# Kernel optimization log

Hardware: AMD Instinct MI355X
Metric: run time of the kernel (lower is better)

## Reference

```python
import jax, jax.numpy as jnp
import numpy as np

B, T, N, H, E, LH, OUT, D = 64, 12, 325, 64, 32, 128, 12, 1
META_OFF = 65  # x[..., :1] is the signal, x[..., 65:] is the 32-dim temporal meta input


def _mlp(meta, W1, b1, W2, b2):
    # meta: (B,E); W1: (4,E,LH); W2: (4,LH,O) -> (4,B,O); 4 = gates g,i,f,o
    h = jax.nn.relu(jnp.einsum('be,geh->gbh', meta, W1) + b1[:, None, :])
    return jnp.einsum('gbh,gho->gbo', h, W2) + b2[:, None, :]


def setup_inputs() -> dict:
    key = jax.random.key(0)
    ks = jax.random.split(key, 16)
    s = lambda k, shape: jax.random.normal(k, shape, dtype=jnp.float32) * 0.05
    return {
        'x': jax.random.normal(ks[0], (B, T, N, 1 + 64 + E), dtype=jnp.float32),
        'lwx_W1': s(ks[1], (4, E, LH)), 'lwx_b1': s(ks[2], (4, LH)),
        'lwx_W2': s(ks[3], (4, LH, D * H)), 'lwx_b2': s(ks[4], (4, D * H)),
        'lwh_W1': s(ks[5], (4, E, LH)), 'lwh_b1': s(ks[6], (4, LH)),
        'lwh_W2': s(ks[7], (4, LH, H * H)), 'lwh_b2': s(ks[8], (4, H * H)),
        'lb_W1': s(ks[9], (4, E, LH)), 'lb_b1': s(ks[10], (4, LH)),
        'lb_W2': s(ks[11], (4, LH, H)), 'lb_b2': s(ks[12], (4, H)),
        'fc1_W': s(ks[13], (H, H // 2)), 'fc1_b': jnp.zeros((H // 2,), jnp.float32),
        'fc2_W': s(ks[14], (H // 2, OUT * D)), 'fc2_b': jnp.zeros((OUT * D,), jnp.float32),
    }


def reference(x, lwx_W1, lwx_b1, lwx_W2, lwx_b2,
              lwh_W1, lwh_b1, lwh_W2, lwh_b2,
              lb_W1, lb_b1, lb_W2, lb_b2,
              fc1_W, fc1_b, fc2_W, fc2_b):
    batch = x.shape[0]
    meta = jnp.mean(x[:, :, 0, META_OFF:], axis=1)  # (B,E)
    xs = jnp.transpose(x[..., :D], (1, 0, 2, 3))    # (T,B,N,D)

    Wx = _mlp(meta, lwx_W1, lwx_b1, lwx_W2, lwx_b2).reshape(4, batch, D, H)
    Wh = _mlp(meta, lwh_W1, lwh_b1, lwh_W2, lwh_b2).reshape(4, batch, H, H)
    b = _mlp(meta, lb_W1, lb_b1, lb_W2, lb_b2).reshape(4, batch, 1, H)

    def step(carry, xt):
        h, c = carry
        # (4,B,N,H): per-batch weights -> batched matmuls for all 4 gates
        z = (jnp.einsum('bnd,gbdh->gbnh', xt, Wx)
             + jnp.einsum('bnh,gbhk->gbnk', h, Wh) + b)
        g = jnp.tanh(z[0])
        i = jax.nn.sigmoid(z[1])
        f = jax.nn.sigmoid(z[2])
        o = jax.nn.sigmoid(z[3])
        c = g * i + c * f
        h = jnp.tanh(c) * o
        return (h, c), None

    # h0=c0=0 reproduces the torch t==0 special case exactly
    h0 = jnp.zeros((batch, N, H), x.dtype)
    (h, _), _ = jax.lax.scan(step, (h0, h0), xs)

    out = jax.nn.relu(h)
    out = jax.nn.relu(out @ fc1_W + fc1_b) @ fc2_W + fc2_b  # (B,N,OUT*D)
    out = out.reshape(batch, N, OUT, D)
    return jnp.transpose(out, (0, 2, 1, 3))  # (B,OUT,N,D)
```

## Files before the change

### kernel.cpp

```cpp
#include <hip/hip_runtime.h>
#include <stdint.h>

#define TT 12
#define NN 325
#define HH 64
#define EE 32
#define LHH 128
#define OO 12
#define CIN 97
#define MOFF 65
#define BB 64

typedef __attribute__((ext_vector_type(8))) short bf8;
typedef __attribute__((ext_vector_type(4))) float f4;

__device__ __forceinline__ float sigf(float x) {
  return __builtin_amdgcn_rcpf(1.f + __builtin_amdgcn_exp2f(-1.4426950408889634f * x));
}
__device__ __forceinline__ float tanhfast(float x) {
  return 1.f - 2.f * __builtin_amdgcn_rcpf(1.f + __builtin_amdgcn_exp2f(2.8853900817779268f * x));
}
__device__ __forceinline__ unsigned short f2bf(float f) {
  unsigned int u = __float_as_uint(f);
  u += 0x7fffu + ((u >> 16) & 1u);
  return (unsigned short)(u >> 16);
}
__device__ __forceinline__ float bf2f(unsigned short s) {
  return __uint_as_float(((unsigned int)s) << 16);
}

__global__ __launch_bounds__(256, 2) void k_prep(
    const float* __restrict__ x,
    const float* __restrict__ xw1, const float* __restrict__ xb1,
    const float* __restrict__ xw2, const float* __restrict__ xb2,
    const float* __restrict__ hw1, const float* __restrict__ hb1,
    const float* __restrict__ hw2, const float* __restrict__ hb2,
    const float* __restrict__ bw1, const float* __restrict__ bb1,
    const float* __restrict__ bw2, const float* __restrict__ bb2,
    unsigned short* __restrict__ whb, float* __restrict__ xg,
    float* __restrict__ wx_ws, float* __restrict__ bg_ws)
{
  const int bi = blockIdx.x, tid = threadIdx.x;
  __shared__ float meta_s[BB][EE];
  __shared__ float hs[BB][132];
  __shared__ float w2s[LHH][HH];

  for (int m = tid; m < BB * EE; m += 256) {
    const int b = m >> 5, e = m & 31;
    float s = 0.f;
    #pragma unroll
    for (int t = 0; t < TT; ++t)
      s += x[(size_t)((b * TT + t) * NN) * CIN + MOFF + e];
    meta_s[b][e] = s * (1.f / 12.f);
  }

  if (bi < 256) {
    const int g = bi >> 6, i = bi & 63;

    const int base = bi * 976;
    #pragma unroll
    for (int kk = 0; kk < 4; ++kk) {
      const int flat = base + kk * 256 + tid;
      if (flat < BB * TT * NN) {
        const int b = flat / (TT * NN);
        const int r = flat - b * (TT * NN);
        const int t = r / NN;
        const int n = r - t * NN;
        xg[flat] = x[(size_t)((b * TT + t) * NN + n) * CIN];
      }
    }
    for (int idx = tid; idx < LHH * HH; idx += 256)
      w2s[idx >> 6][idx & 63] = hw2[(size_t)(g * LHH + (idx >> 6)) * 4096 + i * 64 + (idx & 63)];
    __syncthreads();

    for (int m = tid; m < BB * LHH; m += 256) {
      const int b = m >> 7, l = m & 127;
      float a = hb1[g * LHH + l];
      const float* w = hw1 + (size_t)g * (EE * LHH) + l;
      #pragma unroll
      for (int e = 0; e < EE; ++e) a = fmaf(meta_s[b][e], w[e * LHH], a);
      hs[b][l] = fmaxf(a, 0.f);
    }
    __syncthreads();

    const int rg = tid >> 4, cg = tid & 15;
    const int b0 = rg * 4, j0 = cg * 4;
    float acc[4][4] = {};
    for (int l = 0; l < LHH; l += 4) {
      f4 hv[4];
      #pragma unroll
      for (int rr = 0; rr < 4; ++rr) hv[rr] = *(const f4*)&hs[b0 + rr][l];
      #pragma unroll
      for (int ll = 0; ll < 4; ++ll) {
        const f4 wv = *(const f4*)&w2s[l + ll][j0];
        #pragma unroll
        for (int rr = 0; rr < 4; ++rr)
          #pragma unroll
          for (int jj = 0; jj < 4; ++jj)
            acc[rr][jj] = fmaf(hv[rr][ll], wv[jj], acc[rr][jj]);
      }
    }
    const int kh = i >> 5, quad = (i >> 3) & 3, j8 = i & 7;
    #pragma unroll
    for (int rr = 0; rr < 4; ++rr) {
      const int b = b0 + rr;
      #pragma unroll
      for (int jj = 0; jj < 4; ++jj) {
        const int j = j0 + jj;
        const float v = acc[rr][jj] + hb2[g * 4096 + i * 64 + j];
        const int col = g * 64 + j;
        const int nt = col >> 4, c16 = col & 15;
        const int lane = quad * 16 + c16;
        whb[(size_t)((b * 32 + kh * 16 + nt) * 64 + lane) * 8 + j8] = f2bf(v);
      }
    }
  } else {
    const int role = bi - 256;
    const int g = role >> 1;
    const int isb = role & 1;
    const float* W1 = isb ? bw1 : xw1;
    const float* B1 = isb ? bb1 : xb1;
    const float* W2 = isb ? bw2 : xw2;
    const float* B2 = isb ? bb2 : xb2;
    float* dst = isb ? bg_ws : wx_ws;
    __syncthreads();

    for (int m = tid; m < BB * LHH; m += 256) {
      const int b = m >> 7, l = m & 127;
      float a = B1[g * LHH + l];
      const float* w = W1 + (size_t)g * (EE * LHH) + l;
      #pragma unroll
      for (int e = 0; e < EE; ++e) a = fmaf(meta_s[b][e], w[e * LHH], a);
      hs[b][l] = fmaxf(a, 0.f);
    }
    __syncthreads();

    for (int m = tid; m < BB * HH; m += 256) {
      const int b = m >> 6, h = m & 63;
      float a = B2[g * HH + h];
      const float* w = W2 + (size_t)g * (LHH * HH) + h;
      #pragma unroll 8
      for (int l = 0; l < LHH; ++l) a = fmaf(hs[b][l], w[l * HH], a);
      dst[b * 256 + g * 64 + h] = a;
    }
  }
}

__global__ __launch_bounds__(256, 3) void k_lstm(
    const float* __restrict__ xg, const float* __restrict__ wx_ws,
    const float* __restrict__ bg_ws, const unsigned short* __restrict__ whb,
    const float* __restrict__ fc1W, const float* __restrict__ fc1b,
    const float* __restrict__ fc2W, const float* __restrict__ fc2b,
    float* __restrict__ out)
{
  const int rb = blockIdx.x, b = blockIdx.y, tid = threadIdx.x;
  const int wave = tid >> 6, lane = tid & 63, quad = lane >> 4, c16 = lane & 15;
  const int n0 = rb * 32;

  __shared__ __align__(16) unsigned short Hs[2][2][16][72];
  __shared__ float Xs[TT][32];
  __shared__ float fc1s[HH * 32];
  __shared__ float fc2s[32 * OO];
  __shared__ float HIDs[32][36];
  __shared__ float fc1bs[32];
  __shared__ float fc2bs[OO];

  for (int idx = tid; idx < TT * 32; idx += 256) {
    const int t = idx >> 5, r = idx & 31, n = n0 + r;
    Xs[t][r] = (n < NN) ? xg[b * (TT * NN) + t * NN + n] : 0.f;
  }
  for (int idx = tid; idx < HH * 32; idx += 256) fc1s[idx] = fc1W[idx];
  for (int idx = tid; idx < 32 * OO; idx += 256) fc2s[idx] = fc2W[idx];
  if (tid < 32) fc1bs[tid] = fc1b[tid];
  if (tid < OO) fc2bs[tid] = fc2b[tid];

  float wxv[4], bgv[4];
  #pragma unroll
  for (int g = 0; g < 4; ++g) {
    wxv[g] = wx_ws[b * 256 + g * 64 + wave * 16 + c16];
    bgv[g] = bg_ws[b * 256 + g * 64 + wave * 16 + c16];
  }
  bf8 wf[2][4];
  #pragma unroll
  for (int kh = 0; kh < 2; ++kh)
    #pragma unroll
    for (int g = 0; g < 4; ++g)
      wf[kh][g] = *(const bf8*)(whb + (size_t)((b * 32 + kh * 16 + g * 4 + wave) * 64 + lane) * 8);

  float cst[2][4];
  #pragma unroll
  for (int ta = 0; ta < 2; ++ta)
    #pragma unroll
    for (int r = 0; r < 4; ++r) cst[ta][r] = 0.f;

  __syncthreads();

  #pragma unroll 1
  for (int t = 0; t < TT; ++t) {
    bf8 af[2][2];
    if (t > 0) {
      #pragma unroll
      for (int ta = 0; ta < 2; ++ta) {
        af[ta][0] = *(const bf8*)&Hs[(t - 1) & 1][ta][c16][quad * 8];
        af[ta][1] = *(const bf8*)&Hs[(t - 1) & 1][ta][c16][32 + quad * 8];
      }
    }
    f4 ac[2][4];
    #pragma unroll
    for (int ta = 0; ta < 2; ++ta) {
      float xr[4];
      #pragma unroll
      for (int r = 0; r < 4; ++r) xr[r] = Xs[t][ta * 16 + quad * 4 + r];
      #pragma unroll
      for (int g = 0; g < 4; ++g)
        #pragma unroll
        for (int r = 0; r < 4; ++r)
          ac[ta][g][r] = fmaf(xr[r], wxv[g], bgv[g]);
    }
    if (t > 0) {
      #pragma unroll
      for (int ta = 0; ta < 2; ++ta)
        #pragma unroll
        for (int g = 0; g < 4; ++g) {
          ac[ta][g] = __builtin_amdgcn_mfma_f32_16x16x32_bf16(af[ta][0], wf[0][g], ac[ta][g], 0, 0, 0);
          ac[ta][g] = __builtin_amdgcn_mfma_f32_16x16x32_bf16(af[ta][1], wf[1][g], ac[ta][g], 0, 0, 0);
        }
    }
    #pragma unroll
    for (int ta = 0; ta < 2; ++ta)
      #pragma unroll
      for (int r = 0; r < 4; ++r) {
        const float gg = tanhfast(ac[ta][0][r]);
        const float ii = sigf(ac[ta][1][r]);
        const float ff = sigf(ac[ta][2][r]);
        const float oo = sigf(ac[ta][3][r]);
        const float cc = fmaf(gg, ii, cst[ta][r] * ff);
        cst[ta][r] = cc;
        const float hh = tanhfast(cc) * oo;
        Hs[t & 1][ta][quad * 4 + r][wave * 16 + c16] = f2bf(hh);
      }
    __syncthreads();
  }

  {
    const int row32 = tid & 31, uu = tid >> 5;
    const int ta = row32 >> 4, row = row32 & 15;
    float hacc[4];
    #pragma unroll
    for (int j = 0; j < 4; ++j) hacc[j] = fc1bs[uu * 4 + j];
    #pragma unroll
    for (int kc = 0; kc < 8; ++kc) {
      const bf8 hv = *(const bf8*)&Hs[1][ta][row][kc * 8];
      #pragma unroll
      for (int j8 = 0; j8 < 8; ++j8) {
        const float hk = fmaxf(bf2f((unsigned short)hv[j8]), 0.f);
        const int k = kc * 8 + j8;
        #pragma unroll
        for (int j = 0; j < 4; ++j)
          hacc[j] = fmaf(hk, fc1s[k * 32 + uu * 4 + j], hacc[j]);
      }
    }
    #pragma unroll
    for (int j = 0; j < 4; ++j)
      HIDs[row32][uu * 4 + j] = fmaxf(hacc[j], 0.f);
  }
  __syncthreads();
  for (int idx = tid; idx < 32 * OO; idx += 256) {
    const int o = idx >> 5, row32 = idx & 31;
    float a = fc2bs[o];
    #pragma unroll
    for (int k = 0; k < 32; ++k)
      a = fmaf(HIDs[row32][k], fc2s[k * OO + o], a);
    const int n = n0 + row32;
    if (n < NN)
      out[b * (OO * NN) + o * NN + n] = a;
  }
}

extern "C" void kernel_launch(void* const* d_in, const int* in_sizes, int n_in,
                              void* d_out, int out_size, void* d_ws, size_t ws_size,
                              hipStream_t stream) {
  const float* x    = (const float*)d_in[0];
  const float* xw1  = (const float*)d_in[1];
  const float* xb1  = (const float*)d_in[2];
  const float* xw2  = (const float*)d_in[3];
  const float* xb2  = (const float*)d_in[4];
  const float* hw1  = (const float*)d_in[5];
  const float* hb1  = (const float*)d_in[6];
  const float* hw2  = (const float*)d_in[7];
  const float* hb2  = (const float*)d_in[8];
  const float* bw1  = (const float*)d_in[9];
  const float* bb1  = (const float*)d_in[10];
  const float* bw2  = (const float*)d_in[11];
  const float* bb2  = (const float*)d_in[12];
  const float* fc1W = (const float*)d_in[13];
  const float* fc1b = (const float*)d_in[14];
  const float* fc2W = (const float*)d_in[15];
  const float* fc2b = (const float*)d_in[16];
  float* out = (float*)d_out;

  float* ws = (float*)d_ws;
  float* wx_ws = ws;
  float* bg_ws = ws + 16384;
  float* xg_ws = ws + 32768;
  unsigned short* whb = (unsigned short*)(ws + 32768 + BB * TT * NN);

  k_prep<<<264, 256, 0, stream>>>(x, xw1, xb1, xw2, xb2, hw1, hb1, hw2, hb2,
                                  bw1, bb1, bw2, bb2, whb, xg_ws, wx_ws, bg_ws);
  k_lstm<<<dim3(11, 64), 256, 0, stream>>>(xg_ws, wx_ws, bg_ws, whb,
                                           fc1W, fc1b, fc2W, fc2b, out);
}
```

Before: 247.0 us.

## Split prep kernel to compute meta and hidden MLP layers once

The single prep kernel had each of 264 blocks recompute the full batch meta mean (strided reads of x) and the first hidden MLP layer. The work is now split into two kernels. k_meta runs per batch and computes the meta vector, all first-layer hiddens and the small Wx and bias MLPs. k_wh reads the precomputed Wh hiddens from workspace and does only the large second-layer matmul. This removes redundant strided global reads and recomputation, at the cost of an extra kernel launch and a global round trip for the hidden activations.

```diff
diff --git a/kernel.cpp b/kernel.cpp
--- a/kernel.cpp
+++ b/kernel.cpp
@@ -29,35 +29,81 @@
   return __uint_as_float(((unsigned int)s) << 16);
 }
 
-__global__ __launch_bounds__(256, 2) void k_prep(
+__global__ __launch_bounds__(256) void k_meta(
     const float* __restrict__ x,
     const float* __restrict__ xw1, const float* __restrict__ xb1,
     const float* __restrict__ xw2, const float* __restrict__ xb2,
     const float* __restrict__ hw1, const float* __restrict__ hb1,
-    const float* __restrict__ hw2, const float* __restrict__ hb2,
     const float* __restrict__ bw1, const float* __restrict__ bb1,
     const float* __restrict__ bw2, const float* __restrict__ bb2,
-    unsigned short* __restrict__ whb, float* __restrict__ xg,
-    float* __restrict__ wx_ws, float* __restrict__ bg_ws)
+    float* __restrict__ hid_ws, float* __restrict__ wx_ws,
+    float* __restrict__ bg_ws)
 {
-  const int bi = blockIdx.x, tid = threadIdx.x;
-  __shared__ float meta_s[BB][EE];
+  const int b = blockIdx.x, tid = threadIdx.x;
+  __shared__ float mpart[TT][EE];
+  __shared__ float meta_s[EE];
+  __shared__ float hidx_s[512], hidb_s[512];
+
+  for (int idx = tid; idx < TT * EE; idx += 256) {
+    const int t = idx >> 5, e = idx & 31;
+    mpart[t][e] = x[(size_t)((b * TT + t) * NN) * CIN + MOFF + e];
+  }
+  __syncthreads();
+  if (tid < EE) {
+    float s = 0.f;
+    #pragma unroll
+    for (int t = 0; t < TT; ++t) s += mpart[t][tid];
+    meta_s[tid] = s * (1.f / 12.f);
+  }
+  __syncthreads();
+
+  for (int idx = tid; idx < 1536; idx += 256) {
+    const int mlp = idx >> 9, rem = idx & 511;
+    const int g = rem >> 7, l = rem & 127;
+    const float* W1 = (mlp == 0) ? xw1 : ((mlp == 1) ? hw1 : bw1);
+    const float* B1 = (mlp == 0) ? xb1 : ((mlp == 1) ? hb1 : bb1);
+    float a = B1[rem];
+    const float* w = W1 + g * (EE * LHH) + l;
+    #pragma unroll
+    for (int e = 0; e < EE; ++e) a = fmaf(meta_s[e], w[e * LHH], a);
+    a = fmaxf(a, 0.f);
+    if (mlp == 0) hidx_s[rem] = a;
+    else if (mlp == 2) hidb_s[rem] = a;
+    else hid_ws[g * (BB * LHH) + b * LHH + l] = a;
+  }
+  __syncthreads();
+
+  {
+    const int g = tid >> 6;
+    const int h = tid & 63;
+    float ax = xb2[tid];
+    float ab = bb2[tid];
+    const float* wxp = xw2 + (size_t)g * (LHH * HH) + h;
+    const float* wbp = bw2 + (size_t)g * (LHH * HH) + h;
+    const float* hx = hidx_s + g * LHH;
+    const float* hb = hidb_s + g * LHH;
+    #pragma unroll 8
+    for (int l = 0; l < LHH; ++l) {
+      ax = fmaf(hx[l], wxp[l * HH], ax);
+      ab = fmaf(hb[l], wbp[l * HH], ab);
+    }
+    wx_ws[b * 256 + tid] = ax;
+    bg_ws[b * 256 + tid] = ab;
+  }
+}
+
+__global__ __launch_bounds__(256) void k_wh(
+    const float* __restrict__ x,
+    const float* __restrict__ hw2, const float* __restrict__ hb2,
+    const float* __restrict__ hid_ws, unsigned short* __restrict__ whb,
+    float* __restrict__ xg)
+{
+  const int g = blockIdx.x >> 6, i = blockIdx.x & 63, tid = threadIdx.x;
   __shared__ float hs[BB][132];
   __shared__ float w2s[LHH][HH];
 
-  for (int m = tid; m < BB * EE; m += 256) {
-    const int b = m >> 5, e = m & 31;
-    float s = 0.f;
-    #pragma unroll
-    for (int t = 0; t < TT; ++t)
-      s += x[(size_t)((b * TT + t) * NN) * CIN + MOFF + e];
-    meta_s[b][e] = s * (1.f / 12.f);
-  }
-
-  if (bi < 256) {
-    const int g = bi >> 6, i = bi & 63;
-
-    const int base = bi * 976;
+  {
+    const int base = blockIdx.x * 976;
     #pragma unroll
     for (int kk = 0; kk < 4; ++kk) {
       const int flat = base + kk * 256 + tid;
@@ -69,79 +115,44 @@
         xg[flat] = x[(size_t)((b * TT + t) * NN + n) * CIN];
       }
     }
-    for (int idx = tid; idx < LHH * HH; idx += 256)
-      w2s[idx >> 6][idx & 63] = hw2[(size_t)(g * LHH + (idx >> 6)) * 4096 + i * 64 + (idx & 63)];
-    __syncthreads();
-
-    for (int m = tid; m < BB * LHH; m += 256) {
-      const int b = m >> 7, l = m & 127;
-      float a = hb1[g * LHH + l];
-      const float* w = hw1 + (size_t)g * (EE * LHH) + l;
-      #pragma unroll
-      for (int e = 0; e < EE; ++e) a = fmaf(meta_s[b][e], w[e * LHH], a);
-      hs[b][l] = fmaxf(a, 0.f);
-    }
-    __syncthreads();
-
-    const int rg = tid >> 4, cg = tid & 15;
-    const int b0 = rg * 4, j0 = cg * 4;
-    float acc[4][4] = {};
-    for (int l = 0; l < LHH; l += 4) {
-      f4 hv[4];
-      #pragma unroll
-      for (int rr = 0; rr < 4; ++rr) hv[rr] = *(const f4*)&hs[b0 + rr][l];
-      #pragma unroll
-      for (int ll = 0; ll < 4; ++ll) {
-        const f4 wv = *(const f4*)&w2s[l + ll][j0];
+  }
+
+  for (int idx = tid; idx < BB * LHH; idx += 256)
+    hs[idx >> 7][idx & 127] = hid_ws[g * (BB * LHH) + idx];
+  for (int idx = tid; idx < LHH * HH; idx += 256)
+    w2s[idx >> 6][idx & 63] = hw2[(size_t)(g * LHH + (idx >> 6)) * 4096 + i * 64 + (idx & 63)];
+  __syncthreads();
+
+  const int rg = tid >> 4, cg = tid & 15;
+  const int b0 = rg * 4, j0 = cg * 4;
+  float acc[4][4] = {};
+  for (int l = 0; l < LHH; l += 4) {
+    f4 hv[4];
+    #pragma unroll
+    for (int rr = 0; rr < 4; ++rr) hv[rr] = *(const f4*)&hs[b0 + rr][l];
+    #pragma unroll
+    for (int ll = 0; ll < 4; ++ll) {
+      const f4 wv = *(const f4*)&w2s[l + ll][j0];
+      #pragma unroll
+      for (int rr = 0; rr < 4; ++rr)
         #pragma unroll
-        for (int rr = 0; rr < 4; ++rr)
-          #pragma unroll
-          for (int jj = 0; jj < 4; ++jj)
-            acc[rr][jj] = fmaf(hv[rr][ll], wv[jj], acc[rr][jj]);
-      }
-    }
-    const int kh = i >> 5, quad = (i >> 3) & 3, j8 = i & 7;
-    #pragma unroll
-    for (int rr = 0; rr < 4; ++rr) {
-      const int b = b0 + rr;
-      #pragma unroll
-      for (int jj = 0; jj < 4; ++jj) {
-        const int j = j0 + jj;
-        const float v = acc[rr][jj] + hb2[g * 4096 + i * 64 + j];
-        const int col = g * 64 + j;
-        const int nt = col >> 4, c16 = col & 15;
-        const int lane = quad * 16 + c16;
-        whb[(size_t)((b * 32 + kh * 16 + nt) * 64 + lane) * 8 + j8] = f2bf(v);
-      }
-    }
-  } else {
-    const int role = bi - 256;
-    const int g = role >> 1;
-    const int isb = role & 1;
-    const float* W1 = isb ? bw1 : xw1;
-    const float* B1 = isb ? bb1 : xb1;
-    const float* W2 = isb ? bw2 : xw2;
-    const float* B2 = isb ? bb2 : xb2;
-    float* dst = isb ? bg_ws : wx_ws;
-    __syncthreads();
-
-    for (int m = tid; m < BB * LHH; m += 256) {
-      const int b = m >> 7, l = m & 127;
-      float a = B1[g * LHH + l];
-      const float* w = W1 + (size_t)g * (EE * LHH) + l;
-      #pragma unroll
-      for (int e = 0; e < EE; ++e) a = fmaf(meta_s[b][e], w[e * LHH], a);
-      hs[b][l] = fmaxf(a, 0.f);
-    }
-    __syncthreads();
-
-    for (int m = tid; m < BB * HH; m += 256) {
-      const int b = m >> 6, h = m & 63;
-      float a = B2[g * HH + h];
-      const float* w = W2 + (size_t)g * (LHH * HH) + h;
-      #pragma unroll 8
-      for (int l = 0; l < LHH; ++l) a = fmaf(hs[b][l], w[l * HH], a);
-      dst[b * 256 + g * 64 + h] = a;
+        for (int jj = 0; jj < 4; ++jj)
+          acc[rr][jj] = fmaf(hv[rr][ll], wv[jj], acc[rr][jj]);
+    }
+  }
+
+  const int kh = i >> 5, quad = (i >> 3) & 3, j8 = i & 7;
+  #pragma unroll
+  for (int rr = 0; rr < 4; ++rr) {
+    const int b = b0 + rr;
+    #pragma unroll
+    for (int jj = 0; jj < 4; ++jj) {
+      const int j = j0 + jj;
+      const float v = acc[rr][jj] + hb2[g * 4096 + i * 64 + j];
+      const int col = g * 64 + j;
+      const int nt = col >> 4, c16 = col & 15;
+      const int lane = quad * 16 + c16;
+      whb[(size_t)((b * 32 + kh * 16 + nt) * 64 + lane) * 8 + j8] = f2bf(v);
     }
   }
 }
@@ -300,13 +311,15 @@
   float* out = (float*)d_out;
 
   float* ws = (float*)d_ws;
-  float* wx_ws = ws;
-  float* bg_ws = ws + 16384;
-  float* xg_ws = ws + 32768;
-  unsigned short* whb = (unsigned short*)(ws + 32768 + BB * TT * NN);
-
-  k_prep<<<264, 256, 0, stream>>>(x, xw1, xb1, xw2, xb2, hw1, hb1, hw2, hb2,
-                                  bw1, bb1, bw2, bb2, whb, xg_ws, wx_ws, bg_ws);
+  float* hid_ws = ws;
+  float* wx_ws  = ws + 32768;
+  float* bg_ws  = ws + 49152;
+  float* xg_ws  = ws + 65536;
+  unsigned short* whb = (unsigned short*)(ws + 65536 + BB * TT * NN);
+
+  k_meta<<<64, 256, 0, stream>>>(x, xw1, xb1, xw2, xb2, hw1, hb1, bw1, bb1,
+                                 bw2, bb2, hid_ws, wx_ws, bg_ws);
+  k_wh<<<256, 256, 0, stream>>>(x, hw2, hb2, hid_ws, whb, xg_ws);
   k_lstm<<<dim3(11, 64), 256, 0, stream>>>(xg_ws, wx_ws, bg_ws, whb,
                                            fc1W, fc1b, fc2W, fc2b, out);
 }
```

Measured after the change: 224.5 us. 9.1% less time.

## Split prep MLP work across more blocks and read x signal directly in LSTM

Applied to the files above, without the earlier changes.

The prep kernel now launches 1040 blocks, each handling 16 batches for one gate/row slice. This replaces 264 blocks that each recomputed meta over all 64 batches. The Wh second-layer GEMM now reads weights straight from global memory instead of staging them in shared memory. The Wx and bias MLPs are fused into one block per gate and batch quarter. The separate xg gather buffer is removed, and the LSTM kernel reads the signal channel from x with a strided access. The aim is more parallelism and one less write and read of an intermediate buffer, at the cost of redundant meta and first-layer computation per block and strided global loads.

```diff
diff --git a/kernel.cpp b/kernel.cpp
--- a/kernel.cpp
+++ b/kernel.cpp
@@ -13,6 +13,7 @@
 
 typedef __attribute__((ext_vector_type(8))) short bf8;
 typedef __attribute__((ext_vector_type(4))) float f4;
+typedef __attribute__((ext_vector_type(2))) float f2;
 
 __device__ __forceinline__ float sigf(float x) {
   return __builtin_amdgcn_rcpf(1.f + __builtin_amdgcn_exp2f(-1.4426950408889634f * x));
@@ -29,7 +30,7 @@
   return __uint_as_float(((unsigned int)s) << 16);
 }
 
-__global__ __launch_bounds__(256, 2) void k_prep(
+__global__ __launch_bounds__(256) void k_prep(
     const float* __restrict__ x,
     const float* __restrict__ xw1, const float* __restrict__ xb1,
     const float* __restrict__ xw2, const float* __restrict__ xb2,
@@ -37,75 +38,62 @@
     const float* __restrict__ hw2, const float* __restrict__ hb2,
     const float* __restrict__ bw1, const float* __restrict__ bb1,
     const float* __restrict__ bw2, const float* __restrict__ bb2,
-    unsigned short* __restrict__ whb, float* __restrict__ xg,
+    unsigned short* __restrict__ whb,
     float* __restrict__ wx_ws, float* __restrict__ bg_ws)
 {
   const int bi = blockIdx.x, tid = threadIdx.x;
-  __shared__ float meta_s[BB][EE];
-  __shared__ float hs[BB][132];
-  __shared__ float w2s[LHH][HH];
-
-  for (int m = tid; m < BB * EE; m += 256) {
-    const int b = m >> 5, e = m & 31;
+  const bool gemm = (bi < 1024);
+  const int g  = gemm ? (bi >> 8) : ((bi - 1024) >> 2);
+  const int bq = gemm ? (bi & 3) : ((bi - 1024) & 3);
+
+  __shared__ float meta_s[16][EE];
+  __shared__ float hbuf[2][16][132];
+
+  for (int p = tid; p < 512; p += 256) {
+    const int bl = p >> 5, e = p & 31;
+    const int b = bq * 16 + bl;
     float s = 0.f;
     #pragma unroll
     for (int t = 0; t < TT; ++t)
       s += x[(size_t)((b * TT + t) * NN) * CIN + MOFF + e];
-    meta_s[b][e] = s * (1.f / 12.f);
-  }
-
-  if (bi < 256) {
-    const int g = bi >> 6, i = bi & 63;
-
-    const int base = bi * 976;
-    #pragma unroll
-    for (int kk = 0; kk < 4; ++kk) {
-      const int flat = base + kk * 256 + tid;
-      if (flat < BB * TT * NN) {
-        const int b = flat / (TT * NN);
-        const int r = flat - b * (TT * NN);
-        const int t = r / NN;
-        const int n = r - t * NN;
-        xg[flat] = x[(size_t)((b * TT + t) * NN + n) * CIN];
-      }
-    }
-    for (int idx = tid; idx < LHH * HH; idx += 256)
-      w2s[idx >> 6][idx & 63] = hw2[(size_t)(g * LHH + (idx >> 6)) * 4096 + i * 64 + (idx & 63)];
-    __syncthreads();
-
-    for (int m = tid; m < BB * LHH; m += 256) {
-      const int b = m >> 7, l = m & 127;
+    meta_s[bl][e] = s * (1.f / 12.f);
+  }
+  __syncthreads();
+
+  if (gemm) {
+    const int i = (bi >> 2) & 63;
+    for (int m = tid; m < 16 * LHH; m += 256) {
+      const int bl = m >> 7, l = m & 127;
       float a = hb1[g * LHH + l];
       const float* w = hw1 + (size_t)g * (EE * LHH) + l;
       #pragma unroll
-      for (int e = 0; e < EE; ++e) a = fmaf(meta_s[b][e], w[e * LHH], a);
-      hs[b][l] = fmaxf(a, 0.f);
+      for (int e = 0; e < EE; ++e) a = fmaf(meta_s[bl][e], w[e * LHH], a);
+      hbuf[0][bl][l] = fmaxf(a, 0.f);
     }
     __syncthreads();
 
-    const int rg = tid >> 4, cg = tid & 15;
-    const int b0 = rg * 4, j0 = cg * 4;
-    float acc[4][4] = {};
+    const int r0 = (tid >> 5) * 2, j0 = (tid & 31) * 2;
+    const float* w2p = hw2 + (size_t)(g * LHH) * 4096 + i * 64 + j0;
+    float acc[2][2] = {};
     for (int l = 0; l < LHH; l += 4) {
-      f4 hv[4];
-      #pragma unroll
-      for (int rr = 0; rr < 4; ++rr) hv[rr] = *(const f4*)&hs[b0 + rr][l];
+      const f4 h0 = *(const f4*)&hbuf[0][r0][l];
+      const f4 h1 = *(const f4*)&hbuf[0][r0 + 1][l];
       #pragma unroll
       for (int ll = 0; ll < 4; ++ll) {
-        const f4 wv = *(const f4*)&w2s[l + ll][j0];
-        #pragma unroll
-        for (int rr = 0; rr < 4; ++rr)
-          #pragma unroll
-          for (int jj = 0; jj < 4; ++jj)
-            acc[rr][jj] = fmaf(hv[rr][ll], wv[jj], acc[rr][jj]);
-      }
-    }
+        const f2 wv = *(const f2*)(w2p + (size_t)(l + ll) * 4096);
+        acc[0][0] = fmaf(h0[ll], wv[0], acc[0][0]);
+        acc[0][1] = fmaf(h0[ll], wv[1], acc[0][1]);
+        acc[1][0] = fmaf(h1[ll], wv[0], acc[1][0]);
+        acc[1][1] = fmaf(h1[ll], wv[1], acc[1][1]);
+      }
+    }
+
     const int kh = i >> 5, quad = (i >> 3) & 3, j8 = i & 7;
     #pragma unroll
-    for (int rr = 0; rr < 4; ++rr) {
-      const int b = b0 + rr;
-      #pragma unroll
-      for (int jj = 0; jj < 4; ++jj) {
+    for (int rr = 0; rr < 2; ++rr) {
+      const int b = bq * 16 + r0 + rr;
+      #pragma unroll
+      for (int jj = 0; jj < 2; ++jj) {
         const int j = j0 + jj;
         const float v = acc[rr][jj] + hb2[g * 4096 + i * 64 + j];
         const int col = g * 64 + j;
@@ -115,39 +103,46 @@
       }
     }
   } else {
-    const int role = bi - 256;
-    const int g = role >> 1;
-    const int isb = role & 1;
-    const float* W1 = isb ? bw1 : xw1;
-    const float* B1 = isb ? bb1 : xb1;
-    const float* W2 = isb ? bw2 : xw2;
-    const float* B2 = isb ? bb2 : xb2;
-    float* dst = isb ? bg_ws : wx_ws;
-    __syncthreads();
-
-    for (int m = tid; m < BB * LHH; m += 256) {
-      const int b = m >> 7, l = m & 127;
+    for (int m = tid; m < 2 * 16 * LHH; m += 256) {
+      const int mlp = m >> 11, rem = m & 2047, bl = rem >> 7, l = rem & 127;
+      const float* W1 = mlp ? bw1 : xw1;
+      const float* B1 = mlp ? bb1 : xb1;
       float a = B1[g * LHH + l];
       const float* w = W1 + (size_t)g * (EE * LHH) + l;
       #pragma unroll
-      for (int e = 0; e < EE; ++e) a = fmaf(meta_s[b][e], w[e * LHH], a);
-      hs[b][l] = fmaxf(a, 0.f);
+      for (int e = 0; e < EE; ++e) a = fmaf(meta_s[bl][e], w[e * LHH], a);
+      hbuf[mlp][bl][l] = fmaxf(a, 0.f);
     }
     __syncthreads();
 
-    for (int m = tid; m < BB * HH; m += 256) {
-      const int b = m >> 6, h = m & 63;
-      float a = B2[g * HH + h];
-      const float* w = W2 + (size_t)g * (LHH * HH) + h;
-      #pragma unroll 8
-      for (int l = 0; l < LHH; ++l) a = fmaf(hs[b][l], w[l * HH], a);
-      dst[b * 256 + g * 64 + h] = a;
+    const int h = tid & 63, bl0 = (tid >> 6) * 4;
+    const float* wxp = xw2 + (size_t)g * (LHH * HH) + h;
+    const float* wbp = bw2 + (size_t)g * (LHH * HH) + h;
+    float accx[4], accb[4];
+    #pragma unroll
+    for (int k = 0; k < 4; ++k) {
+      accx[k] = xb2[g * HH + h];
+      accb[k] = bb2[g * HH + h];
+    }
+    for (int l = 0; l < LHH; ++l) {
+      const float wxl = wxp[l * HH], wbl = wbp[l * HH];
+      #pragma unroll
+      for (int k = 0; k < 4; ++k) {
+        accx[k] = fmaf(hbuf[0][bl0 + k][l], wxl, accx[k]);
+        accb[k] = fmaf(hbuf[1][bl0 + k][l], wbl, accb[k]);
+      }
+    }
+    #pragma unroll
+    for (int k = 0; k < 4; ++k) {
+      const int b = bq * 16 + bl0 + k;
+      wx_ws[b * 256 + g * 64 + h] = accx[k];
+      bg_ws[b * 256 + g * 64 + h] = accb[k];
     }
   }
 }
 
 __global__ __launch_bounds__(256, 3) void k_lstm(
-    const float* __restrict__ xg, const float* __restrict__ wx_ws,
+    const float* __restrict__ x, const float* __restrict__ wx_ws,
     const float* __restrict__ bg_ws, const unsigned short* __restrict__ whb,
     const float* __restrict__ fc1W, const float* __restrict__ fc1b,
     const float* __restrict__ fc2W, const float* __restrict__ fc2b,
@@ -167,7 +162,7 @@
 
   for (int idx = tid; idx < TT * 32; idx += 256) {
     const int t = idx >> 5, r = idx & 31, n = n0 + r;
-    Xs[t][r] = (n < NN) ? xg[b * (TT * NN) + t * NN + n] : 0.f;
+    Xs[t][r] = (n < NN) ? x[(size_t)((b * TT + t) * NN + n) * CIN] : 0.f;
   }
   for (int idx = tid; idx < HH * 32; idx += 256) fc1s[idx] = fc1W[idx];
   for (int idx = tid; idx < 32 * OO; idx += 256) fc2s[idx] = fc2W[idx];
@@ -302,11 +297,10 @@
   float* ws = (float*)d_ws;
   float* wx_ws = ws;
   float* bg_ws = ws + 16384;
-  float* xg_ws = ws + 32768;
-  unsigned short* whb = (unsigned short*)(ws + 32768 + BB * TT * NN);
-
-  k_prep<<<264, 256, 0, stream>>>(x, xw1, xb1, xw2, xb2, hw1, hb1, hw2, hb2,
-                                  bw1, bb1, bw2, bb2, whb, xg_ws, wx_ws, bg_ws);
-  k_lstm<<<dim3(11, 64), 256, 0, stream>>>(xg_ws, wx_ws, bg_ws, whb,
+  unsigned short* whb = (unsigned short*)(ws + 32768);
+
+  k_prep<<<1040, 256, 0, stream>>>(x, xw1, xb1, xw2, xb2, hw1, hb1, hw2, hb2,
+                                   bw1, bb1, bw2, bb2, whb, wx_ws, bg_ws);
+  k_lstm<<<dim3(11, 64), 256, 0, stream>>>(x, wx_ws, bg_ws, whb,
                                            fc1W, fc1b, fc2W, fc2b, out);
 }
```

New measurement: 236.7 us. 4.2% less time.
